# Kernel optimization log

Hardware: AMD Instinct MI355X
Metric: run time of the kernel (lower is better)

The kernel has to match this reference:

```python
import jax, jax.numpy as jnp
import numpy as np

B, S, D, K = 64, 2048, 192, 128  # batch, seq, projection_dim, memoryBankSize


def setup_inputs() -> dict:
    key = jax.random.key(0)
    k1, k2, k3 = jax.random.split(key, 3)
    return {
        "projections": jax.random.normal(k1, (B, S, D), jnp.float32),
        "mem_bank": jax.random.normal(k2, (K, D), jnp.float32),
        "glu_w": jax.random.normal(k3, (D, 2 * D), jnp.float32) * 0.05,
        "glu_b": jnp.zeros((2 * D,), jnp.float32),
    }


def _l2_normalize(x, axis):
    # matches tf.math.l2_normalize (eps inside the max under the sqrt)
    sq = jnp.sum(x * x, axis=axis, keepdims=True)
    return x / jnp.sqrt(jnp.maximum(sq, 1e-12))


def _sinkhorn(out):
    # out: [K, N] cosine similarities
    Q = jnp.exp(out / 0.05)
    Kf = jnp.asarray(Q.shape[0], Q.dtype)
    Bf = jnp.asarray(Q.shape[1], Q.dtype)
    Q = Q / jnp.sum(Q)
    for _ in range(3):  # fixed 3 iterations, as in source
        Q = Q / (jnp.sum(Q, axis=1, keepdims=True) * Kf)  # row normalize
        Q = Q / (jnp.sum(Q, axis=0, keepdims=True) * Bf)  # col normalize
    return Q * Bf


def reference(projections, mem_bank, glu_w, glu_b):
    Bsz, Ssz, Dd = projections.shape
    x = projections.reshape(-1, Dd)                      # [N, D]
    proj_n = _l2_normalize(x, axis=1)                    # [N, D]
    mem_n = _l2_normalize(mem_bank, axis=1)              # [K, D]
    sim = jnp.einsum('kd,nd->kn', mem_n, proj_n)         # [K, N]
    Q = _sinkhorn(sim)                                   # [K, N]
    # top_k(Q^T, 1) per token == argmax over codebook axis
    idx = jnp.argmax(Q, axis=0)                          # [N] int
    assign = mem_bank[idx]                               # gather, [N, D]
    # GLU: Dense(2D) then value * sigmoid(gate)
    lin = assign @ glu_w + glu_b                         # [N, 2D]
    gated = lin[:, :Dd] * jax.nn.sigmoid(lin[:, Dd:])    # [N, D]
    # reduce_mean over the stacked pair == average
    return (projections + gated.reshape(Bsz, Ssz, Dd)) * 0.5
```

## Files before the change

### kernel.cpp

```cpp
#include <hip/hip_runtime.h>

#define NTOK  131072
#define DDIM  192
#define KMEM  128
#define TWOD  384
#define SIMBLK 2048
#define CVBLK  1024

typedef _Float16 half8 __attribute__((ext_vector_type(8)));
typedef float   floatx4 __attribute__((ext_vector_type(4)));

__global__ __launch_bounds__(192) void prep_kernel(
    const float* __restrict__ mb, const float* __restrict__ W,
    const float* __restrict__ bias, _Float16* __restrict__ bhi,
    _Float16* __restrict__ blo, float* __restrict__ tab) {
  __shared__ float row[DDIM];
  __shared__ float red[DDIM];
  __shared__ float s_rn;
  const int k = blockIdx.x;
  const int t = threadIdx.x;
  float m = mb[k * DDIM + t];
  row[t] = m;
  red[t] = m * m;
  __syncthreads();
  if (t == 0) {
    float s = 0.f;
    for (int i = 0; i < DDIM; ++i) s += red[i];
    s_rn = 1.0f / sqrtf(fmaxf(s, 1e-12f));
  }
  __syncthreads();
  const float mn = m * s_rn;
  const _Float16 hh = (_Float16)mn;
  const float lo = (mn - (float)hh) * 4096.0f;
  bhi[k * DDIM + t] = hh;
  blo[k * DDIM + t] = (_Float16)lo;
  float a = bias[t], g = bias[DDIM + t];
  for (int d = 0; d < DDIM; ++d) {
    float r = row[d];
    a = fmaf(r, W[d * TWOD + t], a);
    g = fmaf(r, W[d * TWOD + DDIM + t], g);
  }
  float sg = 1.0f / (1.0f + expf(-g));
  tab[k * DDIM + t] = a * sg;
}

#define LSTR 200
__global__ __launch_bounds__(256, 3) void sim_kernel(
    const float* __restrict__ proj, const _Float16* __restrict__ bhi_g,
    const _Float16* __restrict__ blo_g, float* __restrict__ E,
    double* __restrict__ RpT) {
  __shared__ _Float16 Ahi[64 * LSTR];
  __shared__ _Float16 Alo[64 * LSTR];
  __shared__ float rn_s[64];
  const int tid = threadIdx.x;
  const int lane = tid & 63;
  const int wid = tid >> 6;
  const long n0 = (long)blockIdx.x * 64;

  {
    const int row = tid >> 2;
    const int part = tid & 3;
    const float* src = &proj[(n0 + row) * DDIM + part * 48];
    const int lb0 = row * LSTR + part * 48;
    float nsq = 0.f;
#pragma unroll
    for (int i = 0; i < 6; ++i) {
      float4 p0 = *(const float4*)(src + i * 8);
      float4 p1 = *(const float4*)(src + i * 8 + 4);
      float xs[8] = {p0.x, p0.y, p0.z, p0.w, p1.x, p1.y, p1.z, p1.w};
      half8 h, l;
#pragma unroll
      for (int j = 0; j < 8; ++j) {
        float x = xs[j];
        nsq = fmaf(x, x, nsq);
        _Float16 hh = (_Float16)x;
        h[j] = hh;
        l[j] = (_Float16)((x - (float)hh) * 4096.0f);
      }
      *(half8*)&Ahi[lb0 + i * 8] = h;
      *(half8*)&Alo[lb0 + i * 8] = l;
    }
    nsq += __shfl_xor(nsq, 1);
    nsq += __shfl_xor(nsq, 2);
    if (part == 0) rn_s[row] = 1.0f / sqrtf(fmaxf(nsq, 1e-12f));
  }
  __syncthreads();

  const int m_row = lane & 15;
  const int quad = lane >> 4;
  const int code_base = wid * 32;

  float rnv[16];
#pragma unroll
  for (int sm = 0; sm < 4; ++sm)
#pragma unroll
    for (int r = 0; r < 4; ++r) rnv[sm * 4 + r] = rn_s[sm * 16 + quad * 4 + r];

  float rcol[2] = {0.f, 0.f};
#pragma unroll
  for (int sn = 0; sn < 2; ++sn) {
    const int code = code_base + sn * 16 + m_row;
    half8 bh[6], bl[6];
#pragma unroll
    for (int c = 0; c < 6; ++c) {
      const int gb = code * DDIM + c * 32 + quad * 8;
      bh[c] = *(const half8*)&bhi_g[gb];
      bl[c] = *(const half8*)&blo_g[gb];
    }
#pragma unroll
    for (int sm = 0; sm < 4; ++sm) {
      floatx4 a1 = (floatx4)0.0f;
      floatx4 a2 = (floatx4)0.0f;
#pragma unroll
      for (int c = 0; c < 6; ++c) {
        const int ar = (sm * 16 + m_row) * LSTR + c * 32 + quad * 8;
        half8 ah = *(const half8*)&Ahi[ar];
        half8 al = *(const half8*)&Alo[ar];
        a1 = __builtin_amdgcn_mfma_f32_16x16x32_f16(ah, bh[c], a1, 0, 0, 0);
        a2 = __builtin_amdgcn_mfma_f32_16x16x32_f16(ah, bl[c], a2, 0, 0, 0);
        a2 = __builtin_amdgcn_mfma_f32_16x16x32_f16(al, bh[c], a2, 0, 0, 0);
      }
#pragma unroll
      for (int r = 0; r < 4; ++r) {
        const int tok = sm * 16 + quad * 4 + r;
        const float sim = fmaf(a2[r], 0.000244140625f, a1[r]) * rnv[sm * 4 + r];
        const float e = expf(sim / 0.05f);
        E[(n0 + tok) * KMEM + code] = e;
        rcol[sn] += e;
      }
    }
  }
#pragma unroll
  for (int sn = 0; sn < 2; ++sn) {
    rcol[sn] += __shfl_xor(rcol[sn], 16);
    rcol[sn] += __shfl_xor(rcol[sn], 32);
  }
  if (lane < 16) {
    RpT[(long)(code_base + lane) * SIMBLK + blockIdx.x] = (double)rcol[0];
    RpT[(long)(code_base + 16 + lane) * SIMBLK + blockIdx.x] = (double)rcol[1];
  }
}

__global__ __launch_bounds__(256) void u_kernel(const double* __restrict__ RpT,
                                                float* __restrict__ u,
                                                int width) {
  __shared__ double wred[4];
  const int k = blockIdx.x;
  const int t = threadIdx.x;
  double s = 0.0;
  for (int j = t; j < width; j += 256) s += RpT[(long)k * width + j];
#pragma unroll
  for (int off = 1; off < 64; off <<= 1) s += __shfl_xor(s, off);
  if ((t & 63) == 0) wred[t >> 6] = s;
  __syncthreads();
  if (t == 0)
    u[k] = (float)(1.0 / (128.0 * (wred[0] + wred[1] + wred[2] + wred[3])));
}

__global__ __launch_bounds__(256) void cv_kernel(const float* __restrict__ E,
                                                 const float* __restrict__ u,
                                                 double* __restrict__ RpT) {
  __shared__ double part[4][KMEM];
  const int tid = threadIdx.x;
  const int l = tid & 7;
  const int ts = tid >> 3;
  const long n0 = (long)blockIdx.x * 128;
  float4 u4[4];
#pragma unroll
  for (int j = 0; j < 4; ++j) u4[j] = *(const float4*)&u[l * 16 + j * 4];
  double r[16];
#pragma unroll
  for (int i = 0; i < 16; ++i) r[i] = 0.0;
#pragma unroll
  for (int it = 0; it < 4; ++it) {
    const long n = n0 + it * 32 + ts;
    const float* Er = &E[n * KMEM + l * 16];
    const float4 e0 = *(const float4*)(Er + 0);
    const float4 e1 = *(const float4*)(Er + 4);
    const float4 e2 = *(const float4*)(Er + 8);
    const float4 e3 = *(const float4*)(Er + 12);
    double c = (double)e0.x * u4[0].x + (double)e0.y * u4[0].y +
               (double)e0.z * u4[0].z + (double)e0.w * u4[0].w +
               (double)e1.x * u4[1].x + (double)e1.y * u4[1].y +
               (double)e1.z * u4[1].z + (double)e1.w * u4[1].w +
               (double)e2.x * u4[2].x + (double)e2.y * u4[2].y +
               (double)e2.z * u4[2].z + (double)e2.w * u4[2].w +
               (double)e3.x * u4[3].x + (double)e3.y * u4[3].y +
               (double)e3.z * u4[3].z + (double)e3.w * u4[3].w;
    c += __shfl_xor(c, 1);
    c += __shfl_xor(c, 2);
    c += __shfl_xor(c, 4);
    const float v = (float)(1.0 / (131072.0 * c));
    r[0] += (double)(e0.x * v);
    r[1] += (double)(e0.y * v);
    r[2] += (double)(e0.z * v);
    r[3] += (double)(e0.w * v);
    r[4] += (double)(e1.x * v);
    r[5] += (double)(e1.y * v);
    r[6] += (double)(e1.z * v);
    r[7] += (double)(e1.w * v);
    r[8] += (double)(e2.x * v);
    r[9] += (double)(e2.y * v);
    r[10] += (double)(e2.z * v);
    r[11] += (double)(e2.w * v);
    r[12] += (double)(e3.x * v);
    r[13] += (double)(e3.y * v);
    r[14] += (double)(e3.z * v);
    r[15] += (double)(e3.w * v);
  }
#pragma unroll
  for (int i = 0; i < 16; ++i) {
    r[i] += __shfl_xor(r[i], 8);
    r[i] += __shfl_xor(r[i], 16);
    r[i] += __shfl_xor(r[i], 32);
  }
  if ((tid & 63) < 8) {
    const int w = tid >> 6;
#pragma unroll
    for (int i = 0; i < 16; ++i) part[w][l * 16 + i] = r[i];
  }
  __syncthreads();
  if (tid < KMEM) {
    const double s = part[0][tid] + part[1][tid] + part[2][tid] + part[3][tid];
    RpT[(long)tid * CVBLK + blockIdx.x] = s;
  }
}

__global__ __launch_bounds__(256) void argmax_kernel(
    const float* __restrict__ E, const float* __restrict__ u,
    int* __restrict__ idx) {
  const int tid = threadIdx.x;
  const int l = tid & 7;
  const int ts = tid >> 3;
  const long n0 = (long)blockIdx.x * 128;
  float4 u4[4];
#pragma unroll
  for (int j = 0; j < 4; ++j) u4[j] = *(const float4*)&u[l * 16 + j * 4];
#pragma unroll
  for (int it = 0; it < 4; ++it) {
    const long n = n0 + it * 32 + ts;
    const float* Er = &E[n * KMEM + l * 16];
    const float4 e0 = *(const float4*)(Er + 0);
    const float4 e1 = *(const float4*)(Er + 4);
    const float4 e2 = *(const float4*)(Er + 8);
    const float4 e3 = *(const float4*)(Er + 12);
    float p[16];
    p[0] = e0.x * u4[0].x; p[1] = e0.y * u4[0].y;
    p[2] = e0.z * u4[0].z; p[3] = e0.w * u4[0].w;
    p[4] = e1.x * u4[1].x; p[5] = e1.y * u4[1].y;
    p[6] = e1.z * u4[1].z; p[7] = e1.w * u4[1].w;
    p[8] = e2.x * u4[2].x; p[9] = e2.y * u4[2].y;
    p[10] = e2.z * u4[2].z; p[11] = e2.w * u4[2].w;
    p[12] = e3.x * u4[3].x; p[13] = e3.y * u4[3].y;
    p[14] = e3.z * u4[3].z; p[15] = e3.w * u4[3].w;
    float bv = p[0];
    int bi = l * 16;
#pragma unroll
    for (int i = 1; i < 16; ++i) {
      if (p[i] > bv) { bv = p[i]; bi = l * 16 + i; }
    }
#pragma unroll
    for (int off = 1; off < 8; off <<= 1) {
      const float ov = __shfl_xor(bv, off);
      const int oi = __shfl_xor(bi, off);
      if (ov > bv || (ov == bv && oi < bi)) { bv = ov; bi = oi; }
    }
    if (l == 0) idx[n] = bi;
  }
}

__global__ __launch_bounds__(256) void out_kernel(
    const float* __restrict__ proj, const float* __restrict__ tab,
    const int* __restrict__ idx, float* __restrict__ out) {
  const long base = (long)blockIdx.x * 3072;
#pragma unroll
  for (int j = 0; j < 12; ++j) {
    const long f = base + j * 256 + threadIdx.x;
    const int t = (int)(f / 48);
    const int r = (int)(f - (long)t * 48);
    const int id = idx[t];
    const float4 p = *(const float4*)&proj[f * 4];
    const float4 tb = *(const float4*)&tab[id * DDIM + r * 4];
    float4 o;
    o.x = (p.x + tb.x) * 0.5f;
    o.y = (p.y + tb.y) * 0.5f;
    o.z = (p.z + tb.z) * 0.5f;
    o.w = (p.w + tb.w) * 0.5f;
    *(float4*)&out[f * 4] = o;
  }
}

extern "C" void kernel_launch(void* const* d_in, const int* in_sizes, int n_in,
                              void* d_out, int out_size, void* d_ws,
                              size_t ws_size, hipStream_t stream) {
  const float* proj = (const float*)d_in[0];
  const float* mb = (const float*)d_in[1];
  const float* W = (const float*)d_in[2];
  const float* bias = (const float*)d_in[3];
  float* out = (float*)d_out;
  char* ws = (char*)d_ws;
  float* tab = (float*)(ws);
  _Float16* bhi = (_Float16*)(ws + 98304);
  _Float16* blo = (_Float16*)(ws + 147456);
  float* u1 = (float*)(ws + 196608);
  float* u2 = (float*)(ws + 197120);
  float* u3 = (float*)(ws + 197632);
  int* idx = (int*)(ws + 198144);
  double* RpA = (double*)(ws + 722432);
  double* RpB = (double*)(ws + 2819584);
  float* E = out;

  prep_kernel<<<KMEM, DDIM, 0, stream>>>(mb, W, bias, bhi, blo, tab);
  sim_kernel<<<SIMBLK, 256, 0, stream>>>(proj, bhi, blo, E, RpA);
  u_kernel<<<KMEM, 256, 0, stream>>>(RpA, u1, SIMBLK);
  cv_kernel<<<CVBLK, 256, 0, stream>>>(E, u1, RpB);
  u_kernel<<<KMEM, 256, 0, stream>>>(RpB, u2, CVBLK);
  cv_kernel<<<CVBLK, 256, 0, stream>>>(E, u2, RpB);
  u_kernel<<<KMEM, 256, 0, stream>>>(RpB, u3, CVBLK);
  argmax_kernel<<<CVBLK, 256, 0, stream>>>(E, u3, idx);
  out_kernel<<<2048, 256, 0, stream>>>(proj, tab, idx, out);
}
```

Baseline: 296.5 us.

## Swizzle LDS tiles, hoist B fragments, double cv/argmax grids, transpose partials

The sim kernel now loads both code-tile B fragments into registers up front and loops over token sub-tiles, so each A fragment is read from LDS once and reused across both code tiles. Padded LDS rows are replaced with an XOR swizzle to avoid bank conflicts. cv and argmax now use 2048 blocks of 64 tokens instead of 1024 blocks of 128, which raises parallelism. Partial sums are stored block-major, so the u kernel reads them with a strided gather over a fixed count. The cv dot product is summed as a tree, and the extra live registers could cut occupancy in the sim kernel.

```diff
diff --git a/kernel.cpp b/kernel.cpp
--- a/kernel.cpp
+++ b/kernel.cpp
@@ -4,11 +4,14 @@
 #define DDIM  192
 #define KMEM  128
 #define TWOD  384
-#define SIMBLK 2048
-#define CVBLK  1024
+#define GBLK  2048
 
 typedef _Float16 half8 __attribute__((ext_vector_type(8)));
 typedef float   floatx4 __attribute__((ext_vector_type(4)));
+
+__device__ __forceinline__ int swz(int row, int h) {
+  return row * DDIM + ((((h >> 3) ^ (row & 7)) << 3));
+}
 
 __global__ __launch_bounds__(192) void prep_kernel(
     const float* __restrict__ mb, const float* __restrict__ W,
@@ -44,24 +47,37 @@
   tab[k * DDIM + t] = a * sg;
 }
 
-#define LSTR 200
 __global__ __launch_bounds__(256, 3) void sim_kernel(
     const float* __restrict__ proj, const _Float16* __restrict__ bhi_g,
     const _Float16* __restrict__ blo_g, float* __restrict__ E,
-    double* __restrict__ RpT) {
-  __shared__ _Float16 Ahi[64 * LSTR];
-  __shared__ _Float16 Alo[64 * LSTR];
+    double* __restrict__ Rp) {
+  __shared__ _Float16 Ahi[64 * DDIM];
+  __shared__ _Float16 Alo[64 * DDIM];
   __shared__ float rn_s[64];
   const int tid = threadIdx.x;
   const int lane = tid & 63;
   const int wid = tid >> 6;
   const long n0 = (long)blockIdx.x * 64;
+  const int m_row = lane & 15;
+  const int quad = lane >> 4;
+  const int code_base = wid * 32;
+
+  half8 bh[2][6], bl[2][6];
+#pragma unroll
+  for (int sn = 0; sn < 2; ++sn) {
+    const int code = code_base + sn * 16 + m_row;
+#pragma unroll
+    for (int c = 0; c < 6; ++c) {
+      const int gb = code * DDIM + c * 32 + quad * 8;
+      bh[sn][c] = *(const half8*)&bhi_g[gb];
+      bl[sn][c] = *(const half8*)&blo_g[gb];
+    }
+  }
 
   {
     const int row = tid >> 2;
     const int part = tid & 3;
     const float* src = &proj[(n0 + row) * DDIM + part * 48];
-    const int lb0 = row * LSTR + part * 48;
     float nsq = 0.f;
 #pragma unroll
     for (int i = 0; i < 6; ++i) {
@@ -77,8 +93,9 @@
         h[j] = hh;
         l[j] = (_Float16)((x - (float)hh) * 4096.0f);
       }
-      *(half8*)&Ahi[lb0 + i * 8] = h;
-      *(half8*)&Alo[lb0 + i * 8] = l;
+      const int ha = swz(row, part * 48 + i * 8);
+      *(half8*)&Ahi[ha] = h;
+      *(half8*)&Alo[ha] = l;
     }
     nsq += __shfl_xor(nsq, 1);
     nsq += __shfl_xor(nsq, 2);
@@ -86,44 +103,39 @@
   }
   __syncthreads();
 
-  const int m_row = lane & 15;
-  const int quad = lane >> 4;
-  const int code_base = wid * 32;
-
-  float rnv[16];
-#pragma unroll
-  for (int sm = 0; sm < 4; ++sm)
-#pragma unroll
-    for (int r = 0; r < 4; ++r) rnv[sm * 4 + r] = rn_s[sm * 16 + quad * 4 + r];
-
   float rcol[2] = {0.f, 0.f};
 #pragma unroll
-  for (int sn = 0; sn < 2; ++sn) {
-    const int code = code_base + sn * 16 + m_row;
-    half8 bh[6], bl[6];
+  for (int sm = 0; sm < 4; ++sm) {
+    const int arow = sm * 16 + m_row;
+    half8 ah[6], al[6];
 #pragma unroll
     for (int c = 0; c < 6; ++c) {
-      const int gb = code * DDIM + c * 32 + quad * 8;
-      bh[c] = *(const half8*)&bhi_g[gb];
-      bl[c] = *(const half8*)&blo_g[gb];
-    }
-#pragma unroll
-    for (int sm = 0; sm < 4; ++sm) {
-      floatx4 a1 = (floatx4)0.0f;
-      floatx4 a2 = (floatx4)0.0f;
+      const int ha = swz(arow, c * 32 + quad * 8);
+      ah[c] = *(const half8*)&Ahi[ha];
+      al[c] = *(const half8*)&Alo[ha];
+    }
+    floatx4 a1[2], a2[2];
+#pragma unroll
+    for (int sn = 0; sn < 2; ++sn) {
+      a1[sn] = (floatx4)0.0f;
+      a2[sn] = (floatx4)0.0f;
 #pragma unroll
       for (int c = 0; c < 6; ++c) {
-        const int ar = (sm * 16 + m_row) * LSTR + c * 32 + quad * 8;
-        half8 ah = *(const half8*)&Ahi[ar];
-        half8 al = *(const half8*)&Alo[ar];
-        a1 = __builtin_amdgcn_mfma_f32_16x16x32_f16(ah, bh[c], a1, 0, 0, 0);
-        a2 = __builtin_amdgcn_mfma_f32_16x16x32_f16(ah, bl[c], a2, 0, 0, 0);
-        a2 = __builtin_amdgcn_mfma_f32_16x16x32_f16(al, bh[c], a2, 0, 0, 0);
+        a1[sn] = __builtin_amdgcn_mfma_f32_16x16x32_f16(ah[c], bh[sn][c], a1[sn], 0, 0, 0);
+        a2[sn] = __builtin_amdgcn_mfma_f32_16x16x32_f16(ah[c], bl[sn][c], a2[sn], 0, 0, 0);
+        a2[sn] = __builtin_amdgcn_mfma_f32_16x16x32_f16(al[c], bh[sn][c], a2[sn], 0, 0, 0);
       }
+    }
+    float rnr[4];
+#pragma unroll
+    for (int r = 0; r < 4; ++r) rnr[r] = rn_s[sm * 16 + quad * 4 + r];
+#pragma unroll
+    for (int sn = 0; sn < 2; ++sn) {
+      const int code = code_base + sn * 16 + m_row;
 #pragma unroll
       for (int r = 0; r < 4; ++r) {
         const int tok = sm * 16 + quad * 4 + r;
-        const float sim = fmaf(a2[r], 0.000244140625f, a1[r]) * rnv[sm * 4 + r];
+        const float sim = fmaf(a2[sn][r], 0.000244140625f, a1[sn][r]) * rnr[r];
         const float e = expf(sim / 0.05f);
         E[(n0 + tok) * KMEM + code] = e;
         rcol[sn] += e;
@@ -136,19 +148,20 @@
     rcol[sn] += __shfl_xor(rcol[sn], 32);
   }
   if (lane < 16) {
-    RpT[(long)(code_base + lane) * SIMBLK + blockIdx.x] = (double)rcol[0];
-    RpT[(long)(code_base + 16 + lane) * SIMBLK + blockIdx.x] = (double)rcol[1];
-  }
-}
-
-__global__ __launch_bounds__(256) void u_kernel(const double* __restrict__ RpT,
-                                                float* __restrict__ u,
-                                                int width) {
+    Rp[(long)blockIdx.x * KMEM + code_base + lane] = (double)rcol[0];
+    Rp[(long)blockIdx.x * KMEM + code_base + 16 + lane] = (double)rcol[1];
+  }
+}
+
+__global__ __launch_bounds__(256) void u_kernel(const double* __restrict__ Rp,
+                                                float* __restrict__ u) {
   __shared__ double wred[4];
   const int k = blockIdx.x;
   const int t = threadIdx.x;
   double s = 0.0;
-  for (int j = t; j < width; j += 256) s += RpT[(long)k * width + j];
+#pragma unroll
+  for (int j = 0; j < GBLK / 256; ++j)
+    s += Rp[(long)(j * 256 + t) * KMEM + k];
 #pragma unroll
   for (int off = 1; off < 64; off <<= 1) s += __shfl_xor(s, off);
   if ((t & 63) == 0) wred[t >> 6] = s;
@@ -159,12 +172,12 @@
 
 __global__ __launch_bounds__(256) void cv_kernel(const float* __restrict__ E,
                                                  const float* __restrict__ u,
-                                                 double* __restrict__ RpT) {
+                                                 double* __restrict__ Rp) {
   __shared__ double part[4][KMEM];
   const int tid = threadIdx.x;
   const int l = tid & 7;
   const int ts = tid >> 3;
-  const long n0 = (long)blockIdx.x * 128;
+  const long n0 = (long)blockIdx.x * 64;
   float4 u4[4];
 #pragma unroll
   for (int j = 0; j < 4; ++j) u4[j] = *(const float4*)&u[l * 16 + j * 4];
@@ -172,21 +185,23 @@
 #pragma unroll
   for (int i = 0; i < 16; ++i) r[i] = 0.0;
 #pragma unroll
-  for (int it = 0; it < 4; ++it) {
+  for (int it = 0; it < 2; ++it) {
     const long n = n0 + it * 32 + ts;
     const float* Er = &E[n * KMEM + l * 16];
     const float4 e0 = *(const float4*)(Er + 0);
     const float4 e1 = *(const float4*)(Er + 4);
     const float4 e2 = *(const float4*)(Er + 8);
     const float4 e3 = *(const float4*)(Er + 12);
-    double c = (double)e0.x * u4[0].x + (double)e0.y * u4[0].y +
-               (double)e0.z * u4[0].z + (double)e0.w * u4[0].w +
-               (double)e1.x * u4[1].x + (double)e1.y * u4[1].y +
-               (double)e1.z * u4[1].z + (double)e1.w * u4[1].w +
-               (double)e2.x * u4[2].x + (double)e2.y * u4[2].y +
-               (double)e2.z * u4[2].z + (double)e2.w * u4[2].w +
-               (double)e3.x * u4[3].x + (double)e3.y * u4[3].y +
-               (double)e3.z * u4[3].z + (double)e3.w * u4[3].w;
+    double p0 = (double)e0.x * u4[0].x + (double)e0.y * u4[0].y;
+    double p1 = (double)e0.z * u4[0].z + (double)e0.w * u4[0].w;
+    double p2 = (double)e1.x * u4[1].x + (double)e1.y * u4[1].y;
+    double p3 = (double)e1.z * u4[1].z + (double)e1.w * u4[1].w;
+    double p4 = (double)e2.x * u4[2].x + (double)e2.y * u4[2].y;
+    double p5 = (double)e2.z * u4[2].z + (double)e2.w * u4[2].w;
+    double p6 = (double)e3.x * u4[3].x + (double)e3.y * u4[3].y;
+    double p7 = (double)e3.z * u4[3].z + (double)e3.w * u4[3].w;
+    double q0 = p0 + p1, q1 = p2 + p3, q2 = p4 + p5, q3 = p6 + p7;
+    double c = (q0 + q1) + (q2 + q3);
     c += __shfl_xor(c, 1);
     c += __shfl_xor(c, 2);
     c += __shfl_xor(c, 4);
@@ -222,7 +237,7 @@
   __syncthreads();
   if (tid < KMEM) {
     const double s = part[0][tid] + part[1][tid] + part[2][tid] + part[3][tid];
-    RpT[(long)tid * CVBLK + blockIdx.x] = s;
+    Rp[(long)blockIdx.x * KMEM + tid] = s;
   }
 }
 
@@ -232,12 +247,12 @@
   const int tid = threadIdx.x;
   const int l = tid & 7;
   const int ts = tid >> 3;
-  const long n0 = (long)blockIdx.x * 128;
+  const long n0 = (long)blockIdx.x * 64;
   float4 u4[4];
 #pragma unroll
   for (int j = 0; j < 4; ++j) u4[j] = *(const float4*)&u[l * 16 + j * 4];
 #pragma unroll
-  for (int it = 0; it < 4; ++it) {
+  for (int it = 0; it < 2; ++it) {
     const long n = n0 + it * 32 + ts;
     const float* Er = &E[n * KMEM + l * 16];
     const float4 e0 = *(const float4*)(Er + 0);
@@ -311,12 +326,12 @@
   float* E = out;
 
   prep_kernel<<<KMEM, DDIM, 0, stream>>>(mb, W, bias, bhi, blo, tab);
-  sim_kernel<<<SIMBLK, 256, 0, stream>>>(proj, bhi, blo, E, RpA);
-  u_kernel<<<KMEM, 256, 0, stream>>>(RpA, u1, SIMBLK);
-  cv_kernel<<<CVBLK, 256, 0, stream>>>(E, u1, RpB);
-  u_kernel<<<KMEM, 256, 0, stream>>>(RpB, u2, CVBLK);
-  cv_kernel<<<CVBLK, 256, 0, stream>>>(E, u2, RpB);
-  u_kernel<<<KMEM, 256, 0, stream>>>(RpB, u3, CVBLK);
-  argmax_kernel<<<CVBLK, 256, 0, stream>>>(E, u3, idx);
-  out_kernel<<<2048, 256, 0, stream>>>(proj, tab, idx, out);
-}
+  sim_kernel<<<GBLK, 256, 0, stream>>>(proj, bhi, blo, E, RpA);
+  u_kernel<<<KMEM, 256, 0, stream>>>(RpA, u1);
+  cv_kernel<<<GBLK, 256, 0, stream>>>(E, u1, RpB);
+  u_kernel<<<KMEM, 256, 0, stream>>>(RpB, u2);
+  cv_kernel<<<GBLK, 256, 0, stream>>>(E, u2, RpA);
+  u_kernel<<<KMEM, 256, 0, stream>>>(RpA, u3);
+  argmax_kernel<<<GBLK, 256, 0, stream>>>(E, u3, idx);
+  out_kernel<<<GBLK, 256, 0, stream>>>(proj, tab, idx, out);
+}
```

Result: slower. 308.3 us (+4.0%).
